# Performance work log

Hardware: AMD Instinct MI355X
Metric: run time of the kernel (lower is better)

Reference implementation:

```python
import jax, jax.numpy as jnp
import numpy as np

H = 1024      # hidden_dim
S = 32768     # seq_len


def setup_inputs() -> dict:
    key = jax.random.key(0)
    k1, k2, k3, k4, k5 = jax.random.split(key, 5)
    hidden = jax.random.normal(k1, (1, 2 * H), dtype=jnp.float32)
    encoder_output = jax.random.normal(k2, (S, H), dtype=jnp.float32)
    # nn.Linear default init scale ~ 1/sqrt(fan_in)
    attn_w = jax.random.normal(k3, (H, 3 * H), dtype=jnp.float32) / np.sqrt(3 * H)
    attn_b = jax.random.normal(k4, (H,), dtype=jnp.float32) / np.sqrt(3 * H)
    v_w = jax.random.normal(k5, (1, H), dtype=jnp.float32) / np.sqrt(H)
    return {"hidden": hidden, "encoder_output": encoder_output,
            "attn_w": attn_w, "attn_b": attn_b, "v_w": v_w}


def reference(hidden, encoder_output, attn_w, attn_b, v_w):
    seq_len = encoder_output.shape[0]
    h_rep = jnp.broadcast_to(hidden, (seq_len, hidden.shape[1]))  # repeat(seq_len, 1)
    cat = jnp.concatenate([h_rep, encoder_output], axis=1)        # [S, 3H]
    energy = jnp.tanh(cat @ attn_w.T + attn_b)                    # [S, H]
    attention = (energy @ v_w.T).squeeze()                        # [S]
    return jax.nn.softmax(attention, axis=0)
```

## Files before the change

### kernel.cpp

```cpp
#include <hip/hip_runtime.h>
#include <hip/hip_bf16.h>

#define H  1024
#define S  32768
#define H2 2048
#define H3 3072

typedef __attribute__((ext_vector_type(8))) short bf16x8;
typedef __attribute__((ext_vector_type(4))) float f32x4;

__device__ __forceinline__ unsigned short f2bf(float f) {
    unsigned u = __float_as_uint(f);
    u += 0x7fffu + ((u >> 16) & 1u);
    return (unsigned short)(u >> 16);
}

__device__ __forceinline__ unsigned cvt_pk(float lo, float hi) {
    __hip_bfloat162 h = __float22bfloat162_rn(make_float2(lo, hi));
    unsigned u;
    __builtin_memcpy(&u, &h, 4);
    return u;
}

__device__ __forceinline__ float tanh_fast(float x) {
    float e = __expf(2.0f * x);
    return 1.0f - 2.0f / (e + 1.0f);
}

__device__ __forceinline__ void async_copy16(const void* g, void* l) {
    __builtin_amdgcn_global_load_lds(
        (const __attribute__((address_space(1))) unsigned int*)g,
        (__attribute__((address_space(3))) unsigned int*)l,
        16, 0, 0);
}

__global__ void prep_all(const float* __restrict__ enc, const float* __restrict__ attn_w,
                         const float* __restrict__ attn_b, const float* __restrict__ hidden,
                         unsigned short* __restrict__ ebf, unsigned short* __restrict__ w2b,
                         float* __restrict__ dvec, int do_enc) {
    int b = blockIdx.x;
    if (do_enc) {
        if (b < 32768) {
            size_t idx4 = (size_t)b * 256 + threadIdx.x;
            float4 f = ((const float4*)enc)[idx4];
            ushort4 u;
            u.x = f2bf(f.x); u.y = f2bf(f.y); u.z = f2bf(f.z); u.w = f2bf(f.w);
            ((ushort4*)ebf)[idx4] = u;
            return;
        }
        b -= 32768;
    }
    if (b < 1024) {
        int idx4 = b * 256 + threadIdx.x;
        int n = idx4 >> 8;
        int c = (idx4 & 255) * 4;
        float4 f = *(const float4*)(attn_w + (size_t)n * H3 + H2 + c);
        ushort4 u;
        u.x = f2bf(f.x); u.y = f2bf(f.y); u.z = f2bf(f.z); u.w = f2bf(f.w);
        *(ushort4*)(w2b + (size_t)n * H + c) = u;
        return;
    }
    b -= 1024;
    int wv = threadIdx.x >> 6, lane = threadIdx.x & 63;
    int row = b * 4 + wv;
    const float* wrow = attn_w + (size_t)row * H3;
    float s = 0.f;
    #pragma unroll
    for (int j = 0; j < 32; ++j) {
        int k = lane + j * 64;
        s += wrow[k] * hidden[k];
    }
    #pragma unroll
    for (int m = 1; m <= 32; m <<= 1) s += __shfl_xor(s, m);
    if (lane == 0) dvec[row] = s + attn_b[row];
}

__device__ __forceinline__ void epilogue(const f32x4 acc[4][4], const float* __restrict__ dvec,
                                         const float* __restrict__ vw, float* __restrict__ logits,
                                         int rowBlock, int colBlock, int waveM, int waveN,
                                         int quad, int l16) {
    float rowsum[4][4];
    #pragma unroll
    for (int mi = 0; mi < 4; ++mi)
        #pragma unroll
        for (int r = 0; r < 4; ++r) rowsum[mi][r] = 0.f;

    #pragma unroll
    for (int ni = 0; ni < 4; ++ni) {
        int colg = colBlock * 128 + waveN * 64 + ni * 16 + l16;
        float dv = dvec[colg];
        float vv = vw[colg];
        #pragma unroll
        for (int mi = 0; mi < 4; ++mi)
            #pragma unroll
            for (int r = 0; r < 4; ++r)
                rowsum[mi][r] += tanh_fast(acc[mi][ni][r] + dv) * vv;
    }

    #pragma unroll
    for (int mi = 0; mi < 4; ++mi)
        #pragma unroll
        for (int r = 0; r < 4; ++r) {
            float s = rowsum[mi][r];
            s += __shfl_xor(s, 1);
            s += __shfl_xor(s, 2);
            s += __shfl_xor(s, 4);
            s += __shfl_xor(s, 8);
            rowsum[mi][r] = s;
        }

    if (l16 == 0) {
        int rbase = rowBlock * 128 + waveM * 64 + quad * 4;
        #pragma unroll
        for (int mi = 0; mi < 4; ++mi)
            #pragma unroll
            for (int r = 0; r < 4; ++r)
                atomicAdd(&logits[rbase + mi * 16 + r], rowsum[mi][r]);
    }
}

__global__ __launch_bounds__(256, 2) void attn_gemm_fast(
        const unsigned short* __restrict__ ebf, const unsigned short* __restrict__ w2b,
        const float* __restrict__ dvec, const float* __restrict__ vw,
        float* __restrict__ logits) {
    __shared__ unsigned short Atile[128 * 32];
    __shared__ unsigned short Btile[128 * 32];

    const int tid = threadIdx.x;
    const int rowBlock = blockIdx.x & 255;
    const int colBlock = blockIdx.x >> 8;

    const int lane = tid & 63;
    const int wv = tid >> 6;
    const int waveM = wv >> 1, waveN = wv & 1;
    const int quad = lane >> 4, l16 = lane & 15;

    f32x4 acc[4][4];
    #pragma unroll
    for (int mi = 0; mi < 4; ++mi)
        #pragma unroll
        for (int ni = 0; ni < 4; ++ni)
            acc[mi][ni] = (f32x4){0.f, 0.f, 0.f, 0.f};

    const unsigned short* Abase = Atile + (waveM * 64 + l16) * 32 + quad * 8;
    const unsigned short* Bbase = Btile + (waveN * 64 + l16) * 32 + quad * 8;

    const size_t aRow0 = (size_t)(rowBlock * 128) * H;
    const size_t bRow0 = (size_t)(colBlock * 128) * H;

    for (int kt = 0; kt < 32; ++kt) {
        const int k0 = kt * 32;

        #pragma unroll
        for (int p = 0; p < 2; ++p) {
            int c = p * 256 + tid;
            int n = c >> 2, kk = (c & 3) * 8;
            async_copy16(ebf + aRow0 + (size_t)n * H + k0 + kk, (char*)Atile + (size_t)c * 16);
            async_copy16(w2b + bRow0 + (size_t)n * H + k0 + kk, (char*)Btile + (size_t)c * 16);
        }

        __syncthreads();

        bf16x8 af[4], bfr[4];
        #pragma unroll
        for (int i = 0; i < 4; ++i) {
            af[i]  = *(const bf16x8*)(Abase + i * 16 * 32);
            bfr[i] = *(const bf16x8*)(Bbase + i * 16 * 32);
        }
        #pragma unroll
        for (int mi = 0; mi < 4; ++mi)
            #pragma unroll
            for (int ni = 0; ni < 4; ++ni)
                acc[mi][ni] = __builtin_amdgcn_mfma_f32_16x16x32_bf16(
                    af[mi], bfr[ni], acc[mi][ni], 0, 0, 0);

        __syncthreads();
    }

    epilogue(acc, dvec, vw, logits, rowBlock, colBlock, waveM, waveN, quad, l16);
}

__global__ __launch_bounds__(256, 2) void attn_gemm_fb(
        const float* __restrict__ enc, const unsigned short* __restrict__ w2b,
        const float* __restrict__ dvec, const float* __restrict__ vw,
        float* __restrict__ logits) {
    __shared__ unsigned short Atile[128 * 32];
    __shared__ unsigned short Btile[128 * 32];

    const int tid = threadIdx.x;
    const int rowBlock = blockIdx.x & 255;
    const int colBlock = blockIdx.x >> 8;

    const int lane = tid & 63;
    const int wv = tid >> 6;
    const int waveM = wv >> 1, waveN = wv & 1;
    const int quad = lane >> 4, l16 = lane & 15;

    f32x4 acc[4][4];
    #pragma unroll
    for (int mi = 0; mi < 4; ++mi)
        #pragma unroll
        for (int ni = 0; ni < 4; ++ni)
            acc[mi][ni] = (f32x4){0.f, 0.f, 0.f, 0.f};

    const int arow = tid >> 3;
    const int akc  = (tid & 7) * 4;
    const size_t encRowBase = (size_t)(rowBlock * 128) * H;

    const unsigned short* Abase = Atile + (waveM * 64 + l16) * 32 + quad * 8;
    const unsigned short* Bbase = Btile + (waveN * 64 + l16) * 32 + quad * 8;

    for (int kt = 0; kt < 32; ++kt) {
        const int k0 = kt * 32;
        #pragma unroll
        for (int p = 0; p < 2; ++p) {
            int c = p * 256 + tid;
            int n = c >> 2, kk = (c & 3) * 8;
            async_copy16(w2b + (size_t)(colBlock * 128 + n) * H + k0 + kk,
                         (char*)Btile + (size_t)c * 16);
        }
        float4 av[4];
        #pragma unroll
        for (int p = 0; p < 4; ++p)
            av[p] = *(const float4*)(enc + encRowBase + (size_t)(arow + p * 32) * H + k0 + akc);
        #pragma unroll
        for (int p = 0; p < 4; ++p) {
            uint2 u;
            u.x = cvt_pk(av[p].x, av[p].y);
            u.y = cvt_pk(av[p].z, av[p].w);
            *(uint2*)(Atile + (arow + p * 32) * 32 + akc) = u;
        }

        __syncthreads();

        bf16x8 af[4], bfr[4];
        #pragma unroll
        for (int i = 0; i < 4; ++i) {
            af[i]  = *(const bf16x8*)(Abase + i * 16 * 32);
            bfr[i] = *(const bf16x8*)(Bbase + i * 16 * 32);
        }
        #pragma unroll
        for (int mi = 0; mi < 4; ++mi)
            #pragma unroll
            for (int ni = 0; ni < 4; ++ni)
                acc[mi][ni] = __builtin_amdgcn_mfma_f32_16x16x32_bf16(
                    af[mi], bfr[ni], acc[mi][ni], 0, 0, 0);

        __syncthreads();
    }

    epilogue(acc, dvec, vw, logits, rowBlock, colBlock, waveM, waveN, quad, l16);
}

__global__ __launch_bounds__(1024) void softmax_k(float* __restrict__ x) {
    __shared__ float red[16];
    const int tid = threadIdx.x;
    const int lane = tid & 63, wv = tid >> 6;

    float v[32];
    float m = -1e30f;
    #pragma unroll
    for (int i = 0; i < 32; ++i) {
        v[i] = x[tid + (i << 10)];
        m = fmaxf(m, v[i]);
    }
    #pragma unroll
    for (int o = 1; o < 64; o <<= 1) m = fmaxf(m, __shfl_xor(m, o));
    if (lane == 0) red[wv] = m;
    __syncthreads();
    #pragma unroll
    for (int i = 0; i < 16; ++i) m = fmaxf(m, red[i]);
    __syncthreads();

    float s = 0.f;
    #pragma unroll
    for (int i = 0; i < 32; ++i) {
        v[i] = expf(v[i] - m);
        s += v[i];
    }
    #pragma unroll
    for (int o = 1; o < 64; o <<= 1) s += __shfl_xor(s, o);
    if (lane == 0) red[wv] = s;
    __syncthreads();
    float tot = 0.f;
    #pragma unroll
    for (int i = 0; i < 16; ++i) tot += red[i];
    float inv = 1.0f / tot;

    #pragma unroll
    for (int i = 0; i < 32; ++i) x[tid + (i << 10)] = v[i] * inv;
}

extern "C" void kernel_launch(void* const* d_in, const int* in_sizes, int n_in,
                              void* d_out, int out_size, void* d_ws, size_t ws_size,
                              hipStream_t stream) {
    const float* hidden = (const float*)d_in[0];
    const float* enc    = (const float*)d_in[1];
    const float* attn_w = (const float*)d_in[2];
    const float* attn_b = (const float*)d_in[3];
    const float* v_w    = (const float*)d_in[4];
    float* out = (float*)d_out;

    const size_t EBF_BYTES = (size_t)S * H * 2;
    const size_t W2_BYTES  = (size_t)H * H * 2;
    const bool fast = ws_size >= EBF_BYTES + W2_BYTES + 4096;

    hipMemsetAsync(d_out, 0, (size_t)S * sizeof(float), stream);

    if (fast) {
        unsigned short* ebf = (unsigned short*)d_ws;
        unsigned short* w2b = (unsigned short*)((char*)d_ws + EBF_BYTES);
        float* dvec = (float*)((char*)d_ws + EBF_BYTES + W2_BYTES);
        prep_all<<<dim3(32768 + 1024 + 256), dim3(256), 0, stream>>>(
            enc, attn_w, attn_b, hidden, ebf, w2b, dvec, 1);
        attn_gemm_fast<<<dim3(2048), dim3(256), 0, stream>>>(ebf, w2b, dvec, v_w, out);
    } else {
        unsigned short* w2b = (unsigned short*)d_ws;
        float* dvec = (float*)((char*)d_ws + W2_BYTES);
        prep_all<<<dim3(1024 + 256), dim3(256), 0, stream>>>(
            enc, attn_w, attn_b, hidden, nullptr, w2b, dvec, 0);
        attn_gemm_fb<<<dim3(2048), dim3(256), 0, stream>>>(enc, w2b, dvec, v_w, out);
    }
    softmax_k<<<dim3(1), dim3(1024), 0, stream>>>(out);
}
```

Baseline: 312.8 us.

## Widen GEMM K-tile, XOR-swizzle LDS, reorder blocks, fold memset into prep

The fast GEMM now loads 64-wide K tiles, halving the number of barrier-separated iterations, and stores them in LDS with an XOR swizzle to avoid bank conflicts on fragment reads. Block indexing is changed so the 8 column blocks sharing one row block run adjacently, which should improve L2 reuse of the bf16 encoder rows. The separate memset of the output logits moves into extra blocks of the prep kernel, removing one launch. The cost is LDS per block doubling to 32 KB.

```diff
diff --git a/kernel.cpp b/kernel.cpp
--- a/kernel.cpp
+++ b/kernel.cpp
@@ -37,8 +37,13 @@
 __global__ void prep_all(const float* __restrict__ enc, const float* __restrict__ attn_w,
                          const float* __restrict__ attn_b, const float* __restrict__ hidden,
                          unsigned short* __restrict__ ebf, unsigned short* __restrict__ w2b,
-                         float* __restrict__ dvec, int do_enc) {
+                         float* __restrict__ dvec, float* __restrict__ logits, int do_enc) {
     int b = blockIdx.x;
+    if (b < 32) {
+        ((float4*)logits)[b * 256 + threadIdx.x] = (float4){0.f, 0.f, 0.f, 0.f};
+        return;
+    }
+    b -= 32;
     if (do_enc) {
         if (b < 32768) {
             size_t idx4 = (size_t)b * 256 + threadIdx.x;
@@ -123,12 +128,12 @@
         const unsigned short* __restrict__ ebf, const unsigned short* __restrict__ w2b,
         const float* __restrict__ dvec, const float* __restrict__ vw,
         float* __restrict__ logits) {
-    __shared__ unsigned short Atile[128 * 32];
-    __shared__ unsigned short Btile[128 * 32];
+    __shared__ unsigned short Atile[128 * 64];
+    __shared__ unsigned short Btile[128 * 64];
 
     const int tid = threadIdx.x;
-    const int rowBlock = blockIdx.x & 255;
-    const int colBlock = blockIdx.x >> 8;
+    const int colBlock = blockIdx.x & 7;
+    const int rowBlock = blockIdx.x >> 3;
 
     const int lane = tid & 63;
     const int wv = tid >> 6;
@@ -142,37 +147,53 @@
         for (int ni = 0; ni < 4; ++ni)
             acc[mi][ni] = (f32x4){0.f, 0.f, 0.f, 0.f};
 
-    const unsigned short* Abase = Atile + (waveM * 64 + l16) * 32 + quad * 8;
-    const unsigned short* Bbase = Btile + (waveN * 64 + l16) * 32 + quad * 8;
-
     const size_t aRow0 = (size_t)(rowBlock * 128) * H;
     const size_t bRow0 = (size_t)(colBlock * 128) * H;
 
-    for (int kt = 0; kt < 32; ++kt) {
-        const int k0 = kt * 32;
-
-        #pragma unroll
-        for (int p = 0; p < 2; ++p) {
+    int srow[4], sk[4];
+    #pragma unroll
+    for (int p = 0; p < 4; ++p) {
+        int c = p * 256 + tid;
+        srow[p] = c >> 3;
+        sk[p] = ((c & 7) ^ (srow[p] & 7)) * 8;
+    }
+
+    for (int kt = 0; kt < 16; ++kt) {
+        const int k0 = kt * 64;
+
+        #pragma unroll
+        for (int p = 0; p < 4; ++p) {
             int c = p * 256 + tid;
-            int n = c >> 2, kk = (c & 3) * 8;
-            async_copy16(ebf + aRow0 + (size_t)n * H + k0 + kk, (char*)Atile + (size_t)c * 16);
-            async_copy16(w2b + bRow0 + (size_t)n * H + k0 + kk, (char*)Btile + (size_t)c * 16);
+            async_copy16(ebf + aRow0 + (size_t)srow[p] * H + k0 + sk[p],
+                         (char*)Atile + (size_t)c * 16);
+        }
+        #pragma unroll
+        for (int p = 0; p < 4; ++p) {
+            int c = p * 256 + tid;
+            async_copy16(w2b + bRow0 + (size_t)srow[p] * H + k0 + sk[p],
+                         (char*)Btile + (size_t)c * 16);
         }
 
         __syncthreads();
 
-        bf16x8 af[4], bfr[4];
-        #pragma unroll
-        for (int i = 0; i < 4; ++i) {
-            af[i]  = *(const bf16x8*)(Abase + i * 16 * 32);
-            bfr[i] = *(const bf16x8*)(Bbase + i * 16 * 32);
-        }
-        #pragma unroll
-        for (int mi = 0; mi < 4; ++mi)
-            #pragma unroll
-            for (int ni = 0; ni < 4; ++ni)
-                acc[mi][ni] = __builtin_amdgcn_mfma_f32_16x16x32_bf16(
-                    af[mi], bfr[ni], acc[mi][ni], 0, 0, 0);
+        #pragma unroll
+        for (int kk = 0; kk < 2; ++kk) {
+            const int slot = ((kk * 4 + quad) ^ (l16 & 7)) * 16;
+            bf16x8 af[4], bfr[4];
+            #pragma unroll
+            for (int i = 0; i < 4; ++i) {
+                int ar = waveM * 64 + i * 16 + l16;
+                int br = waveN * 64 + i * 16 + l16;
+                af[i]  = *(const bf16x8*)((const char*)Atile + ar * 128 + slot);
+                bfr[i] = *(const bf16x8*)((const char*)Btile + br * 128 + slot);
+            }
+            #pragma unroll
+            for (int mi = 0; mi < 4; ++mi)
+                #pragma unroll
+                for (int ni = 0; ni < 4; ++ni)
+                    acc[mi][ni] = __builtin_amdgcn_mfma_f32_16x16x32_bf16(
+                        af[mi], bfr[ni], acc[mi][ni], 0, 0, 0);
+        }
 
         __syncthreads();
     }
@@ -305,20 +326,18 @@
     const size_t W2_BYTES  = (size_t)H * H * 2;
     const bool fast = ws_size >= EBF_BYTES + W2_BYTES + 4096;
 
-    hipMemsetAsync(d_out, 0, (size_t)S * sizeof(float), stream);
-
     if (fast) {
         unsigned short* ebf = (unsigned short*)d_ws;
         unsigned short* w2b = (unsigned short*)((char*)d_ws + EBF_BYTES);
         float* dvec = (float*)((char*)d_ws + EBF_BYTES + W2_BYTES);
-        prep_all<<<dim3(32768 + 1024 + 256), dim3(256), 0, stream>>>(
-            enc, attn_w, attn_b, hidden, ebf, w2b, dvec, 1);
+        prep_all<<<dim3(32 + 32768 + 1024 + 256), dim3(256), 0, stream>>>(
+            enc, attn_w, attn_b, hidden, ebf, w2b, dvec, out, 1);
         attn_gemm_fast<<<dim3(2048), dim3(256), 0, stream>>>(ebf, w2b, dvec, v_w, out);
     } else {
         unsigned short* w2b = (unsigned short*)d_ws;
         float* dvec = (float*)((char*)d_ws + W2_BYTES);
-        prep_all<<<dim3(1024 + 256), dim3(256), 0, stream>>>(
-            enc, attn_w, attn_b, hidden, nullptr, w2b, dvec, 0);
+        prep_all<<<dim3(32 + 1024 + 256), dim3(256), 0, stream>>>(
+            enc, attn_w, attn_b, hidden, nullptr, w2b, dvec, out, 0);
         attn_gemm_fb<<<dim3(2048), dim3(256), 0, stream>>>(enc, w2b, dvec, v_w, out);
     }
     softmax_k<<<dim3(1), dim3(1024), 0, stream>>>(out);
```

Measured after the change: 307.4 us. Within noise of the previous version (-1.7%).
